# Kernel tuning notes

Measured on AMD Instinct MI355X. Metric: run time of the kernel, lower is better.

Reference implementation:

```python
import jax, jax.numpy as jnp
import numpy as np

B, SD, SE = 4, 2048, 2048
HID, HID_ = 300, 512
N_HEADS = 8


def setup_inputs() -> dict:
    key = jax.random.key(0)
    ks = jax.random.split(key, 7)
    en = jax.random.normal(ks[0], (B, SE, HID), dtype=jnp.float32)
    de = jax.random.normal(ks[1], (B, SD, HID), dtype=jnp.float32)
    mask = jax.random.randint(ks[2], (1, 1, SD, SE), 0, 2).astype(jnp.bool_)
    WQ = jax.random.normal(ks[3], (HID, HID_), dtype=jnp.float32)
    WK = jax.random.normal(ks[4], (HID, HID_), dtype=jnp.float32)
    WV = jax.random.normal(ks[5], (HID, HID_), dtype=jnp.float32)
    WO = jax.random.normal(ks[6], (HID_, HID), dtype=jnp.float32)
    return {"en": en, "de": de, "mask": mask, "WQ": WQ, "WK": WK, "WV": WV, "WO": WO}


def reference(en, de, mask, WQ, WK, WV, WO):
    # Faithful to the torch module (dropout in eval mode => identity).
    d_k = de.shape[-1]  # NOTE: original scales by sqrt(hidden_dim)=sqrt(300), not head_dim
    b_d, s_d = de.shape[0], de.shape[1]
    b_e, s_e = en.shape[0], en.shape[1]
    # head axis is the LAST axis of the reshape (size 8), exactly as the original view/permute
    q = jnp.transpose((de @ WQ).reshape(b_d, s_d, -1, N_HEADS), (3, 0, 1, 2))  # [8,B,Sd,64]
    k = jnp.transpose((en @ WK).reshape(b_e, s_e, -1, N_HEADS), (3, 0, 2, 1))  # [8,B,64,Se]
    v = jnp.transpose((en @ WV).reshape(b_e, s_e, -1, N_HEADS), (3, 0, 1, 2))  # [8,B,Se,64]
    e = jnp.matmul(q, k) / jnp.sqrt(jnp.asarray(d_k, dtype=q.dtype))           # [8,B,Sd,Se]
    e = jnp.where(mask, jnp.asarray(-1e9, dtype=e.dtype), e)
    alpha = jax.nn.softmax(e, axis=3)
    head3 = jnp.matmul(alpha, v)                                               # [8,B,Sd,64]
    # torch.cat((head3[0],...,head3[7]), 2) == move head axis into feature concat order
    a = jnp.concatenate([head3[h] for h in range(N_HEADS)], axis=2)            # [B,Sd,512]
    return a @ WO                                                              # [B,Sd,300]
```

## Files before the change

kernel.cpp:

```cpp
#include <hip/hip_runtime.h>
#include <hip/hip_bf16.h>
#include <math.h>

#define B_      4
#define SD_     2048
#define SE_     2048
#define HIDIN   300
#define HIDMID  512
#define NH      8
#define DH      64
#define ESZ     ((size_t)4194304)
#define BUFB    24576

typedef __attribute__((ext_vector_type(8))) short          s16x8;
typedef __attribute__((ext_vector_type(8))) unsigned short u16x8;
typedef __attribute__((ext_vector_type(4))) unsigned short u16x4;
typedef __attribute__((ext_vector_type(4))) float          f32x4;

#define MFMA16 __builtin_amdgcn_mfma_f32_16x16x32_bf16

#define QSCALE  0.0832940411f
#define NEGL   -1.4426950e9f
#define DEFER_THR 24.0f

__device__ __forceinline__ unsigned short f2bf(float f) {
    unsigned int u = __float_as_uint(f);
    u += 0x7fffu + ((u >> 16) & 1u);
    return (unsigned short)(u >> 16);
}
__device__ __forceinline__ float bf2f(unsigned short s) {
    return __uint_as_float((unsigned int)s << 16);
}
__device__ __forceinline__ void gload16(const void* g, void* l) {
    __builtin_amdgcn_global_load_lds(
        (const __attribute__((address_space(1))) void*)g,
        (__attribute__((address_space(3))) void*)l, 16, 0, 0);
}

#define OF_QH   ((size_t)0)
#define OF_QL   (ESZ)
#define OF_KH   (2*ESZ)
#define OF_KL   (3*ESZ)
#define OF_VT   (4*ESZ)
#define OF_CA   (5*ESZ)
#define OF_CW   (OF_CA + 10485760)
#define OF_WOT  (OF_CW + 983040)

__global__ __launch_bounds__(256) void bias_kernel(const int* __restrict__ mask,
                                                   unsigned int* __restrict__ BiasT)
{
    const int idx = blockIdx.x * 256 + threadIdx.x;
    const int q = idx >> 5, tile = idx & 31;
    const int* __restrict__ mrow = mask + (size_t)q * SE_ + tile * 64;
    const unsigned int NEGB = (unsigned int)f2bf(NEGL);
    const int qblk = q >> 4, qlo = q & 15;
#pragma unroll
    for (int g = 0; g < 4; ++g) {
        unsigned int w[8];
#pragma unroll
        for (int sub = 0; sub < 4; ++sub) {
            const int4 mm = *(const int4*)(mrow + sub * 16 + g * 4);
            w[sub * 2]     = (mm.x ? NEGB : 0u) | ((mm.y ? NEGB : 0u) << 16);
            w[sub * 2 + 1] = (mm.z ? NEGB : 0u) | ((mm.w ? NEGB : 0u) << 16);
        }
        unsigned int* dst = BiasT +
            ((((size_t)qblk * 32 + tile) * 4 + g) * 16 + qlo) * 8;
        *(uint4*)dst       = make_uint4(w[0], w[1], w[2], w[3]);
        *(uint4*)(dst + 4) = make_uint4(w[4], w[5], w[6], w[7]);
    }
}

__global__ __launch_bounds__(256) void convA_kernel(
    const float* __restrict__ de, const float* __restrict__ en,
    unsigned short* __restrict__ CA)
{
    const int idx = blockIdx.x * 256 + threadIdx.x;
    const int mat = blockIdx.y;
    const float* __restrict__ A = mat ? en : de;
    unsigned short* __restrict__ H = CA + (size_t)mat * 5242880;
    unsigned short* __restrict__ L = H + 2621440;
    const int row = idx / 10, ch = idx - row * 10;
    float v[32];
    if (ch < 9) {
#pragma unroll
        for (int i = 0; i < 8; ++i) {
            const float4 f = *(const float4*)(A + (size_t)row * 300 + ch * 32 + i * 4);
            v[i*4+0] = f.x; v[i*4+1] = f.y; v[i*4+2] = f.z; v[i*4+3] = f.w;
        }
    } else {
#pragma unroll
        for (int i = 0; i < 32; ++i) {
            const int k = 288 + i;
            v[i] = (k < 300) ? A[(size_t)row * 300 + k] : 0.f;
        }
    }
    const int r128 = row & 127;
    const int xr = (r128 >> 1) & 3;
    const size_t tb = ((size_t)(row >> 7) * 10 + ch) * 4096 + r128 * 32;
#pragma unroll
    for (int sub = 0; sub < 4; ++sub) {
        const int slot = sub ^ xr;
        u16x8 hv, lv;
#pragma unroll
        for (int e = 0; e < 8; ++e) {
            const float f = v[sub * 8 + e];
            const unsigned short h = f2bf(f);
            hv[e] = h; lv[e] = f2bf(f - bf2f(h));
        }
        *(u16x8*)(H + tb + slot * 8) = hv;
        *(u16x8*)(L + tb + slot * 8) = lv;
    }
}

__global__ __launch_bounds__(256) void convW_kernel(
    const float* __restrict__ WQ, const float* __restrict__ WK,
    const float* __restrict__ WV, const float* __restrict__ WO,
    unsigned short* __restrict__ CW, unsigned short* __restrict__ WOT)
{
    const int idx = blockIdx.x * 256 + threadIdx.x;
    if (idx < 122880) {
        const int which = idx / 40960;
        const int rem = idx - which * 40960;
        const int k = rem >> 7;
        const int n0 = (rem & 127) * 4;
        const float* __restrict__ W = which == 0 ? WQ : (which == 1 ? WK : WV);
        unsigned short* __restrict__ H = CW + (size_t)which * 327680;
        unsigned short* __restrict__ L = H + 163840;
        const float sc = (which == 0) ? QSCALE : 1.f;
        float4 w = make_float4(0.f, 0.f, 0.f, 0.f);
        if (k < 300) w = *(const float4*)(W + (size_t)k * 512 + n0);
        const float wv4[4] = {w.x * sc, w.y * sc, w.z * sc, w.w * sc};
        const int ch = k >> 5, kk = k & 31;
#pragma unroll
        for (int j = 0; j < 4; ++j) {
            const int n = n0 + j, ntile = n >> 7, nr = n & 127;
            const size_t o = ((size_t)(ntile * 10 + ch) * 128 + nr) * 32
                           + (((kk >> 3) ^ ((nr >> 1) & 3)) << 3) + (kk & 7);
            const unsigned short h = f2bf(wv4[j]);
            H[o] = h; L[o] = f2bf(wv4[j] - bf2f(h));
        }
    } else {
        const int idx2 = idx - 122880;
        const int k = idx2 / 96, n4 = idx2 - k * 96;
        const int n0 = n4 * 4;
        float4 w = make_float4(0.f, 0.f, 0.f, 0.f);
        if (n0 < 300) w = *(const float4*)(WO + (size_t)k * 300 + n0);
        const float wv4[4] = {w.x, w.y, w.z, w.w};
        const int ch = k >> 5, kk = k & 31;
#pragma unroll
        for (int j = 0; j < 4; ++j) {
            const int n = n0 + j, ntile = n >> 7, nr = n & 127;
            const size_t o = ((size_t)(ntile * 16 + ch) * 128 + nr) * 32
                           + (((kk >> 3) ^ ((nr >> 1) & 3)) << 3) + (kk & 7);
            WOT[o] = f2bf(wv4[j]);
        }
    }
}

__global__ __launch_bounds__(256) void proj_mfma_kernel(
    const unsigned short* __restrict__ CA, const unsigned short* __restrict__ CW,
    unsigned short* __restrict__ Qh, unsigned short* __restrict__ Ql,
    unsigned short* __restrict__ KhT, unsigned short* __restrict__ KlT,
    unsigned short* __restrict__ VtT)
{
    const int stile = blockIdx.x, jtile = blockIdx.y, which = blockIdx.z;
    const int tid = threadIdx.x, wv = tid >> 6, lane = tid & 63;
    const int li = lane & 15, g = lane >> 4;
    const int wr = wv >> 1, wc = wv & 1;

    __shared__ __align__(16) char LBp[65536];

    const unsigned short* __restrict__ pAh =
        CA + (size_t)(which ? 1 : 0) * 5242880 + (size_t)stile * 40960 + tid * 8;
    const unsigned short* __restrict__ pAl = pAh + 2621440;
    const unsigned short* __restrict__ pWh =
        CW + (size_t)which * 327680 + (size_t)jtile * 40960 + tid * 8;
    const unsigned short* __restrict__ pWl = pWh + 163840;

#define STAGEP(ch, bofs) {                                                    \
        char* db = LBp + (bofs) + wv * 1024;                                  \
        const size_t co = (size_t)(ch) * 4096;                                \
        gload16(pAh + co,        db);                                         \
        gload16(pAh + co + 2048, db + 4096);                                  \
        gload16(pAl + co,        db + 8192);                                  \
        gload16(pAl + co + 2048, db + 12288);                                 \
        gload16(pWh + co,        db + 16384);                                 \
        gload16(pWh + co + 2048, db + 20480);                                 \
        gload16(pWl + co,        db + 24576);                                 \
        gload16(pWl + co + 2048, db + 28672);                                 \
    }

    int offA[4], offW[4];
#pragma unroll
    for (int ssub = 0; ssub < 4; ++ssub) {
        const int r = wr * 64 + ssub * 16 + li;
        offA[ssub] = r * 64 + ((g ^ ((r >> 1) & 3)) << 4);
    }
#pragma unroll
    for (int jsub = 0; jsub < 4; ++jsub) {
        const int n = wc * 64 + jsub * 16 + li;
        offW[jsub] = n * 64 + ((g ^ ((n >> 1) & 3)) << 4);
    }

    f32x4 acc[4][4];
#pragma unroll
    for (int i = 0; i < 4; ++i)
#pragma unroll
        for (int j = 0; j < 4; ++j) acc[i][j] = (f32x4){0.f, 0.f, 0.f, 0.f};

    STAGEP(0, 0)
    __syncthreads();

#pragma unroll 1
    for (int ch = 0; ch < 10; ++ch) {
        const int bofs = (ch & 1) * 32768;
        if (ch < 9) STAGEP(ch + 1, bofs ^ 32768)
        const char* bp = LBp + bofs;
        s16x8 ah[4], al[4], wh[4], wl[4];
#pragma unroll
        for (int ssub = 0; ssub < 4; ++ssub) {
            ah[ssub] = *(const s16x8*)(bp + offA[ssub]);
            al[ssub] = *(const s16x8*)(bp + 8192 + offA[ssub]);
        }
#pragma unroll
        for (int jsub = 0; jsub < 4; ++jsub) {
            wh[jsub] = *(const s16x8*)(bp + 16384 + offW[jsub]);
            wl[jsub] = *(const s16x8*)(bp + 24576 + offW[jsub]);
        }
        __builtin_amdgcn_s_setprio(1);
#pragma unroll
        for (int ssub = 0; ssub < 4; ++ssub)
#pragma unroll
            for (int jsub = 0; jsub < 4; ++jsub) {
                acc[ssub][jsub] = MFMA16(ah[ssub], wh[jsub], acc[ssub][jsub], 0, 0, 0);
                acc[ssub][jsub] = MFMA16(ah[ssub], wl[jsub], acc[ssub][jsub], 0, 0, 0);
                acc[ssub][jsub] = MFMA16(al[ssub], wh[jsub], acc[ssub][jsub], 0, 0, 0);
            }
        __builtin_amdgcn_s_setprio(0);
        __syncthreads();
    }
#undef STAGEP

    const int jgbase = jtile * 128 + wc * 64 + li;
    const int sbase0 = stile * 128 + wr * 64 + 4 * g;
#pragma unroll
    for (int jsub = 0; jsub < 4; ++jsub) {
        const int jgg = jgbase + jsub * 16;
        const int d = jgg >> 3, hh = jgg & 7;
#pragma unroll
        for (int ssub = 0; ssub < 4; ++ssub) {
            const f32x4 v = acc[ssub][jsub];
            const int sg0 = sbase0 + ssub * 16;
            const int bbv = sg0 >> 11;
            const int bhn = bbv * 8 + hh;
            const int sl0 = sg0 & 2047;
            if (which == 0) {
                const size_t o = ((size_t)bhn * 2048 + sl0) * 64 + d;
#pragma unroll
                for (int r = 0; r < 4; ++r) {
                    const float val = v[r];
                    const unsigned short hi = f2bf(val);
                    Qh[o + r * 64] = hi;
                    Ql[o + r * 64] = f2bf(val - bf2f(hi));
                }
            } else if (which == 1) {
                const int tile = sl0 >> 6, tt0 = sl0 & 63;
                const size_t tb = ((size_t)(bhn * 32 + tile)) << 12;
#pragma unroll
                for (int r = 0; r < 4; ++r) {
                    const int tt = tt0 + r;
                    const size_t o = tb + tt * 64 + (((d >> 3) ^ (tt & 7)) << 3) + (d & 7);
                    const float val = v[r];
                    const unsigned short hi = f2bf(val);
                    KhT[o] = hi;
                    KlT[o] = f2bf(val - bf2f(hi));
                }
            } else {
                const int tile = sl0 >> 6, tin0 = sl0 & 63;
                const size_t tb = ((size_t)(bhn * 32 + tile)) << 12;
                const int blk = tin0 >> 5, gg2 = (tin0 >> 2) & 3, half = (tin0 >> 4) & 1;
                const size_t o = tb + (size_t)d * 64
                               + ((((blk << 2) | gg2) ^ (d & 7)) << 3) + half * 4;
                u16x4 pk;
#pragma unroll
                for (int r = 0; r < 4; ++r) pk[r] = f2bf(v[r]);
                *(u16x4*)(VtT + o) = pk;
            }
        }
    }
}

__global__ __launch_bounds__(256, 2) void attn_mfma_kernel(
    const unsigned short* __restrict__ Qh, const unsigned short* __restrict__ Ql,
    const unsigned short* __restrict__ KhT, const unsigned short* __restrict__ KlT,
    const unsigned short* __restrict__ VtT, const unsigned int* __restrict__ BiasT,
    unsigned short* __restrict__ AOb)
{
    const int lin = blockIdx.x + 16 * blockIdx.y;
    const int qt = (lin >> 3) & 15;
    const int bh = (lin & 7) + ((lin >> 7) << 3);
    const int bb = bh >> 3, hh = bh & 7;
    const int tid = threadIdx.x;
    const int wv = tid >> 6, lane = tid & 63;
    const int g = lane >> 4, li = lane & 15;
    const int q0r = qt * 128 + wv * 16 + li;

    __shared__ __align__(16) char LB[3 * BUFB];

    const size_t qoff = ((size_t)bh * SD_ + q0r) * DH + 8 * g;
    const s16x8 qh0_0 = *(const s16x8*)(Qh + qoff);
    const s16x8 qh1_0 = *(const s16x8*)(Qh + qoff + 32);
    const s16x8 ql0_0 = *(const s16x8*)(Ql + qoff);
    const s16x8 ql1_0 = *(const s16x8*)(Ql + qoff + 32);
    const s16x8 qh0_1 = *(const s16x8*)(Qh + qoff + 4096);
    const s16x8 qh1_1 = *(const s16x8*)(Qh + qoff + 4128);
    const s16x8 ql0_1 = *(const s16x8*)(Ql + qoff + 4096);
    const s16x8 ql1_1 = *(const s16x8*)(Ql + qoff + 4128);

    const unsigned short* __restrict__ sKh = KhT + ((size_t)bh << 17) + tid * 8;
    const unsigned short* __restrict__ sKl = KlT + ((size_t)bh << 17) + tid * 8;
    const unsigned short* __restrict__ sVt = VtT + ((size_t)bh << 17) + tid * 8;

    const int base0 = li * 128 + ((g ^ (li & 7)) << 4);
    const int base1 = li * 128 + (((4 + g) ^ (li & 7)) << 4);

    const size_t bb0 = ((((size_t)(qt * 8 + 0 * 4 + wv)) * 32) * 4 + g) * 16 * 8 + li * 8;
    const size_t bb1 = ((((size_t)(qt * 8 + 1 * 4 + wv)) * 32) * 4 + g) * 16 * 8 + li * 8;
#define BIASLOAD(T, R0A, R0B, R1A, R1B) {                                     \
        const uint4* p0 = (const uint4*)(BiasT + bb0 + (size_t)(T) * 512);    \
        R0A = p0[0]; R0B = p0[1];                                             \
        const uint4* p1 = (const uint4*)(BiasT + bb1 + (size_t)(T) * 512);    \
        R1A = p1[0]; R1B = p1[1];                                             \
    }

#define STAGE(tile, boff)                                                     \
    {                                                                         \
        char* db = LB + (boff) + wv * 1024;                                   \
        const size_t toff = (size_t)(tile) << 12;                             \
        gload16(sKh + toff,        db);                                       \
        gload16(sKh + toff + 2048, db + 4096);                                \
        gload16(sKl + toff,        db + 8192);                                \
        gload16(sKl + toff + 2048, db + 12288);                               \
        gload16(sVt + toff,        db + 16384);                               \
        gload16(sVt + toff + 2048, db + 20480);                               \
    }

    float m0 = -INFINITY, m1 = -INFINITY;
    f32x4 O0[4], O1[4], lacc0, lacc1;
#pragma unroll
    for (int i = 0; i < 4; ++i) {
        O0[i] = (f32x4){0.f, 0.f, 0.f, 0.f};
        O1[i] = (f32x4){0.f, 0.f, 0.f, 0.f};
    }
    lacc0 = (f32x4){0.f, 0.f, 0.f, 0.f};
    lacc1 = (f32x4){0.f, 0.f, 0.f, 0.f};

    s16x8 ones;
#pragma unroll
    for (int i = 0; i < 8; ++i) ones[i] = (short)0x3F80;

    uint4 cA0, cA1, cB0, cB1;
    uint4 nA0, nA1, nB0, nB1;

    STAGE(0, 0)
    BIASLOAD(0, cA0, cA1, cB0, cB1)
    STAGE(1, BUFB)
    asm volatile("s_waitcnt vmcnt(6)" ::: "memory");
    __builtin_amdgcn_s_barrier();
    __builtin_amdgcn_sched_barrier(0);

    int cc = 0, cs = 2 * BUFB;

#define UNPK(W, S, sub, cbase)                                                \
        S[sub][cbase]     = __uint_as_float((W) << 16);                       \
        S[sub][cbase + 1] = __uint_as_float((W) & 0xFFFF0000u);

#define ITER(IT, C0A, C0B, C1A, C1B, N0A, N0B, N1A, N1B)                      \
    {                                                                         \
        f32x4 s0[4], s1[4];                                                   \
        UNPK(C0A.x, s0, 0, 0) UNPK(C0A.y, s0, 0, 2)                           \
        UNPK(C0A.z, s0, 1, 0) UNPK(C0A.w, s0, 1, 2)                           \
        UNPK(C0B.x, s0, 2, 0) UNPK(C0B.y, s0, 2, 2)                           \
        UNPK(C0B.z, s0, 3, 0) UNPK(C0B.w, s0, 3, 2)                           \
        UNPK(C1A.x, s1, 0, 0) UNPK(C1A.y, s1, 0, 2)                           \
        UNPK(C1A.z, s1, 1, 0) UNPK(C1A.w, s1, 1, 2)                           \
        UNPK(C1B.x, s1, 2, 0) UNPK(C1B.y, s1, 2, 2)                           \
        UNPK(C1B.z, s1, 3, 0) UNPK(C1B.w, s1, 3, 2)                           \
        BIASLOAD(((IT) + 1) & 31, N0A, N0B, N1A, N1B)                         \
        __builtin_amdgcn_s_setprio(1);                                        \
        _Pragma("unroll")                                                     \
        for (int sub = 0; sub < 4; ++sub) {                                   \
            const s16x8 kh0 = *(const s16x8*)(LB + cc + base0 + sub * 2048);  \
            const s16x8 kh1 = *(const s16x8*)(LB + cc + base1 + sub * 2048);  \
            const s16x8 kl0 = *(const s16x8*)(LB + cc + base0 + 8192 + sub * 2048); \
            const s16x8 kl1 = *(const s16x8*)(LB + cc + base1 + 8192 + sub * 2048); \
            s0[sub] = MFMA16(kh0, qh0_0, s0[sub], 0, 0, 0);                   \
            s0[sub] = MFMA16(kh0, ql0_0, s0[sub], 0, 0, 0);                   \
            s0[sub] = MFMA16(kl0, qh0_0, s0[sub], 0, 0, 0);                   \
            s0[sub] = MFMA16(kh1, qh1_0, s0[sub], 0, 0, 0);                   \
            s0[sub] = MFMA16(kh1, ql1_0, s0[sub], 0, 0, 0);                   \
            s0[sub] = MFMA16(kl1, qh1_0, s0[sub], 0, 0, 0);                   \
            s1[sub] = MFMA16(kh0, qh0_1, s1[sub], 0, 0, 0);                   \
            s1[sub] = MFMA16(kh0, ql0_1, s1[sub], 0, 0, 0);                   \
            s1[sub] = MFMA16(kl0, qh0_1, s1[sub], 0, 0, 0);                   \
            s1[sub] = MFMA16(kh1, qh1_1, s1[sub], 0, 0, 0);                   \
            s1[sub] = MFMA16(kh1, ql1_1, s1[sub], 0, 0, 0);                   \
            s1[sub] = MFMA16(kl1, qh1_1, s1[sub], 0, 0, 0);                   \
        }                                                                     \
        __builtin_amdgcn_s_setprio(0);                                        \
        float t0, t1;                                                         \
        {                                                                     \
            float a = fmaxf(s0[0][0], fmaxf(s0[0][1], s0[0][2]));             \
            float b = fmaxf(s0[0][3], fmaxf(s0[1][0], s0[1][1]));             \
            float c = fmaxf(s0[1][2], fmaxf(s0[1][3], s0[2][0]));             \
            float d = fmaxf(s0[2][1], fmaxf(s0[2][2], s0[2][3]));             \
            float e = fmaxf(s0[3][0], fmaxf(s0[3][1], s0[3][2]));             \
            t0 = fmaxf(fmaxf(a, fmaxf(b, c)), fmaxf(s0[3][3], fmaxf(d, e)));  \
        }                                                                     \
        {                                                                     \
            float a = fmaxf(s1[0][0], fmaxf(s1[0][1], s1[0][2]));             \
            float b = fmaxf(s1[0][3], fmaxf(s1[1][0], s1[1][1]));             \
            float c = fmaxf(s1[1][2], fmaxf(s1[1][3], s1[2][0]));             \
            float d = fmaxf(s1[2][1], fmaxf(s1[2][2], s1[2][3]));             \
            float e = fmaxf(s1[3][0], fmaxf(s1[3][1], s1[3][2]));             \
            t1 = fmaxf(fmaxf(a, fmaxf(b, c)), fmaxf(s1[3][3], fmaxf(d, e)));  \
        }                                                                     \
        const int okd = (t0 <= m0 + DEFER_THR) && (t1 <= m1 + DEFER_THR);     \
        if (!__all(okd)) {                                                    \
            float r0 = fmaxf(t0, __shfl_xor(t0, 16));                         \
            r0 = fmaxf(r0, __shfl_xor(r0, 32));                               \
            float r1 = fmaxf(t1, __shfl_xor(t1, 16));                         \
            r1 = fmaxf(r1, __shfl_xor(r1, 32));                               \
            const float mn0 = fmaxf(m0, r0), mn1 = fmaxf(m1, r1);             \
            const float sc0 = exp2f(m0 - mn0), sc1 = exp2f(m1 - mn1);         \
            m0 = mn0; m1 = mn1;                                               \
            _Pragma("unroll")                                                 \
            for (int i = 0; i < 4; ++i) { O0[i] *= sc0; O1[i] *= sc1; }       \
            lacc0 *= sc0; lacc1 *= sc1;                                       \
        }                                                                     \
        _Pragma("unroll")                                                     \
        for (int sub = 0; sub < 4; ++sub)                                     \
            _Pragma("unroll")                                                 \
            for (int c = 0; c < 4; ++c) {                                     \
                s0[sub][c] = exp2f(s0[sub][c] - m0);                          \
                s1[sub][c] = exp2f(s1[sub][c] - m1);                          \
            }                                                                 \
        union { s16x8 v; unsigned int w[4]; } P00, P10, P01, P11;             \
        asm("v_cvt_pk_bf16_f32 %0, %1, %2" : "=v"(P00.w[0]) : "v"(s0[0][0]), "v"(s0[0][1])); \
        asm("v_cvt_pk_bf16_f32 %0, %1, %2" : "=v"(P00.w[1]) : "v"(s0[0][2]), "v"(s0[0][3])); \
        asm("v_cvt_pk_bf16_f32 %0, %1, %2" : "=v"(P00.w[2]) : "v"(s0[1][0]), "v"(s0[1][1])); \
        asm("v_cvt_pk_bf16_f32 %0, %1, %2" : "=v"(P00.w[3]) : "v"(s0[1][2]), "v"(s0[1][3])); \
        asm("v_cvt_pk_bf16_f32 %0, %1, %2" : "=v"(P10.w[0]) : "v"(s0[2][0]), "v"(s0[2][1])); \
        asm("v_cvt_pk_bf16_f32 %0, %1, %2" : "=v"(P10.w[1]) : "v"(s0[2][2]), "v"(s0[2][3])); \
        asm("v_cvt_pk_bf16_f32 %0, %1, %2" : "=v"(P10.w[2]) : "v"(s0[3][0]), "v"(s0[3][1])); \
        asm("v_cvt_pk_bf16_f32 %0, %1, %2" : "=v"(P10.w[3]) : "v"(s0[3][2]), "v"(s0[3][3])); \
        asm("v_cvt_pk_bf16_f32 %0, %1, %2" : "=v"(P01.w[0]) : "v"(s1[0][0]), "v"(s1[0][1])); \
        asm("v_cvt_pk_bf16_f32 %0, %1, %2" : "=v"(P01.w[1]) : "v"(s1[0][2]), "v"(s1[0][3])); \
        asm("v_cvt_pk_bf16_f32 %0, %1, %2" : "=v"(P01.w[2]) : "v"(s1[1][0]), "v"(s1[1][1])); \
        asm("v_cvt_pk_bf16_f32 %0, %1, %2" : "=v"(P01.w[3]) : "v"(s1[1][2]), "v"(s1[1][3])); \
        asm("v_cvt_pk_bf16_f32 %0, %1, %2" : "=v"(P11.w[0]) : "v"(s1[2][0]), "v"(s1[2][1])); \
        asm("v_cvt_pk_bf16_f32 %0, %1, %2" : "=v"(P11.w[1]) : "v"(s1[2][2]), "v"(s1[2][3])); \
        asm("v_cvt_pk_bf16_f32 %0, %1, %2" : "=v"(P11.w[2]) : "v"(s1[3][0]), "v"(s1[3][1])); \
        asm("v_cvt_pk_bf16_f32 %0, %1, %2" : "=v"(P11.w[3]) : "v"(s1[3][2]), "v"(s1[3][3])); \
        __builtin_amdgcn_s_setprio(1);                                        \
        _Pragma("unroll")                                                     \
        for (int dsub = 0; dsub < 4; ++dsub) {                                \
            const s16x8 vf0 = *(const s16x8*)(LB + cc + base0 + 16384 + dsub * 2048); \
            const s16x8 vf1 = *(const s16x8*)(LB + cc + base1 + 16384 + dsub * 2048); \
            O0[dsub] = MFMA16(vf0, P00.v, O0[dsub], 0, 0, 0);                 \
            O0[dsub] = MFMA16(vf1, P10.v, O0[dsub], 0, 0, 0);                 \
            O1[dsub] = MFMA16(vf0, P01.v, O1[dsub], 0, 0, 0);                 \
            O1[dsub] = MFMA16(vf1, P11.v, O1[dsub], 0, 0, 0);                 \
        }                                                                     \
        lacc0 = MFMA16(ones, P00.v, lacc0, 0, 0, 0);                          \
        lacc0 = MFMA16(ones, P10.v, lacc0, 0, 0, 0);                          \
        lacc1 = MFMA16(ones, P01.v, lacc1, 0, 0, 0);                          \
        lacc1 = MFMA16(ones, P11.v, lacc1, 0, 0, 0);                          \
        __builtin_amdgcn_s_setprio(0);                                        \
        STAGE(((IT) + 2) & 31, cs)                                            \
        asm volatile("s_waitcnt vmcnt(6)" ::: "memory");                      \
        __builtin_amdgcn_s_barrier();                                         \
        __builtin_amdgcn_sched_barrier(0);                                    \
        cc += BUFB; if (cc == 3 * BUFB) cc = 0;                               \
        cs += BUFB; if (cs == 3 * BUFB) cs = 0;                               \
    }

#pragma unroll 1
    for (int itp = 0; itp < 32; itp += 2) {
        ITER(itp,     cA0, cA1, cB0, cB1, nA0, nA1, nB0, nB1)
        ITER(itp + 1, nA0, nA1, nB0, nB1, cA0, cA1, cB0, cB1)
    }

#pragma unroll
    for (int qs = 0; qs < 2; ++qs) {
        const float rl = 1.f / (qs ? lacc1[0] : lacc0[0]);
        const f32x4* Oq = qs ? O1 : O0;
        const int row = bb * 2048 + qt * 128 + qs * 64 + wv * 16 + li;
        const int r128 = row & 127;
        const int xr = (r128 >> 1) & 3;
        unsigned short* __restrict__ ab = AOb + ((size_t)(row >> 7)) * 65536
                                        + r128 * 32 + (g & 1) * 4;
#pragma unroll
        for (int dsub = 0; dsub < 4; ++dsub) {
            const f32x4 o = Oq[dsub] * rl;
            const int ch = hh * 2 + (dsub >> 1);
            const int slot = ((dsub & 1) * 2 + (g >> 1)) ^ xr;
            u16x4 pk;
#pragma unroll
            for (int c = 0; c < 4; ++c) pk[c] = f2bf(o[c]);
            *(u16x4*)(ab + (size_t)ch * 4096 + slot * 8) = pk;
        }
    }
#undef STAGE
#undef BIASLOAD
#undef UNPK
#undef ITER
}

__global__ __launch_bounds__(256) void epi_mfma_kernel(
    const unsigned short* __restrict__ AOb, const unsigned short* __restrict__ WOT,
    float* __restrict__ out)
{
    const int stile = blockIdx.x, jtile = blockIdx.y;
    const int tid = threadIdx.x, wv = tid >> 6, lane = tid & 63;
    const int li = lane & 15, g = lane >> 4;

    __shared__ __align__(16) char LBe[24576];

    const unsigned short* __restrict__ pA =
        AOb + (size_t)(stile >> 1) * 65536 + (stile & 1) * 2048 + tid * 8;
    const unsigned short* __restrict__ pW = WOT + (size_t)jtile * 65536 + tid * 8;

#define STAGEE(ch, bofs) {                                                    \
        char* dbA = LBe + (bofs) + wv * 1024;                                 \
        const size_t co = (size_t)(ch) * 4096;                                \
        gload16(pA + co,        dbA);                                         \
        gload16(pW + co,        dbA + 4096);                                  \
        gload16(pW + co + 2048, dbA + 8192);                                  \
    }

    int offA[4], offW[2];
#pragma unroll
    for (int ssub = 0; ssub < 4; ++ssub) {
        const int r = ssub * 16 + li;
        offA[ssub] = r * 64 + ((g ^ ((r >> 1) & 3)) << 4);
    }
#pragma unroll
    for (int jsub = 0; jsub < 2; ++jsub) {
        const int n = wv * 32 + jsub * 16 + li;
        offW[jsub] = 4096 + n * 64 + ((g ^ ((n >> 1) & 3)) << 4);
    }

    f32x4 acc[4][2];
#pragma unroll
    for (int i = 0; i < 4; ++i)
#pragma unroll
        for (int j = 0; j < 2; ++j) acc[i][j] = (f32x4){0.f, 0.f, 0.f, 0.f};

    STAGEE(0, 0)
    __syncthreads();

#pragma unroll 1
    for (int ch = 0; ch < 16; ++ch) {
        const int bofs = (ch & 1) * 12288;
        if (ch < 15) STAGEE(ch + 1, bofs ^ 12288)
        const char* bp = LBe + bofs;
        s16x8 ah[4], wh[2];
#pragma unroll
        for (int ssub = 0; ssub < 4; ++ssub)
            ah[ssub] = *(const s16x8*)(bp + offA[ssub]);
#pragma unroll
        for (int jsub = 0; jsub < 2; ++jsub)
            wh[jsub] = *(const s16x8*)(bp + offW[jsub]);
        __builtin_amdgcn_s_setprio(1);
#pragma unroll
        for (int ssub = 0; ssub < 4; ++ssub)
#pragma unroll
            for (int jsub = 0; jsub < 2; ++jsub)
                acc[ssub][jsub] = MFMA16(ah[ssub], wh[jsub], acc[ssub][jsub], 0, 0, 0);
        __builtin_amdgcn_s_setprio(0);
        __syncthreads();
    }
#undef STAGEE

    const int nbase = jtile * 128 + wv * 32 + li;
    const int rbase = stile * 64 + 4 * g;
#pragma unroll
    for (int jsub = 0; jsub < 2; ++jsub) {
        const int o = nbase + jsub * 16;
        if (o < HIDIN) {
#pragma unroll
            for (int ssub = 0; ssub < 4; ++ssub) {
                const f32x4 v = acc[ssub][jsub];
                const int r0 = rbase + ssub * 16;
#pragma unroll
                for (int r = 0; r < 4; ++r)
                    out[(size_t)(r0 + r) * HIDIN + o] = v[r];
            }
        }
    }
}

extern "C" void kernel_launch(void* const* d_in, const int* in_sizes, int n_in,
                              void* d_out, int out_size, void* d_ws, size_t ws_size,
                              hipStream_t stream)
{
    const float* en  = (const float*)d_in[0];
    const float* de  = (const float*)d_in[1];
    const int*   mask = (const int*)d_in[2];
    const float* WQ  = (const float*)d_in[3];
    const float* WK  = (const float*)d_in[4];
    const float* WV  = (const float*)d_in[5];
    const float* WO  = (const float*)d_in[6];
    float* out = (float*)d_out;

    unsigned short* ws2 = (unsigned short*)d_ws;
    unsigned short* Qh  = ws2 + OF_QH;
    unsigned short* Ql  = ws2 + OF_QL;
    unsigned short* KhT = ws2 + OF_KH;
    unsigned short* KlT = ws2 + OF_KL;
    unsigned short* VtT = ws2 + OF_VT;
    unsigned short* CA  = ws2 + OF_CA;
    unsigned short* CW  = ws2 + OF_CW;
    unsigned short* WOT = ws2 + OF_WOT;
    unsigned short* AOb = CA;
    unsigned int*  BiasT = (unsigned int*)(CA + 4194304);

    convA_kernel<<<dim3(320, 2), 256, 0, stream>>>(de, en, CA);
    convW_kernel<<<dim3(672), 256, 0, stream>>>(WQ, WK, WV, WO, CW, WOT);
    proj_mfma_kernel<<<dim3(64, 4, 3), 256, 0, stream>>>(CA, CW, Qh, Ql, KhT, KlT, VtT);
    bias_kernel<<<dim3(256), 256, 0, stream>>>(mask, BiasT);
    attn_mfma_kernel<<<dim3(16, 32), 256, 0, stream>>>(Qh, Ql, KhT, KlT, VtT, BiasT, AOb);
    epi_mfma_kernel<<<dim3(128, 3), 256, 0, stream>>>(AOb, WOT, out);
}
```

Measured before the change: 187.8 us.

## Double attention block to 8 waves and software-pipeline QK with softmax-PV

The attention kernel now uses 512-thread blocks covering 256 query rows, so each staged K/V tile in LDS is shared by twice as many waves, and the LDS ring grows from three to four buffers. The loop is software-pipelined so the QK^T MFMAs for tile i+1 are issued alongside the softmax and PV work for tile i, with a prologue and epilogue added. The aim is to halve K/V global traffic per query and hide the exp/convert latency behind tensor-core work. In exchange it needs more registers for two live score sets and more LDS, which may lower occupancy below the two blocks per CU requested.

```diff
diff --git a/kernel.cpp b/kernel.cpp
--- a/kernel.cpp
+++ b/kernel.cpp
@@ -290,32 +290,33 @@
     }
 }
 
-__global__ __launch_bounds__(256, 2) void attn_mfma_kernel(
+__global__ __launch_bounds__(512, 2) void attn_mfma_kernel(
     const unsigned short* __restrict__ Qh, const unsigned short* __restrict__ Ql,
     const unsigned short* __restrict__ KhT, const unsigned short* __restrict__ KlT,
     const unsigned short* __restrict__ VtT, const unsigned int* __restrict__ BiasT,
     unsigned short* __restrict__ AOb)
 {
-    const int lin = blockIdx.x + 16 * blockIdx.y;
-    const int qt = (lin >> 3) & 15;
-    const int bh = (lin & 7) + ((lin >> 7) << 3);
+    const int lin = blockIdx.x + 8 * blockIdx.y;
+    const int j = lin >> 3;
+    const int qt = j & 7;
+    const int bh = (lin & 7) + ((j >> 3) << 3);
     const int bb = bh >> 3, hh = bh & 7;
     const int tid = threadIdx.x;
     const int wv = tid >> 6, lane = tid & 63;
     const int g = lane >> 4, li = lane & 15;
-    const int q0r = qt * 128 + wv * 16 + li;
-
-    __shared__ __align__(16) char LB[3 * BUFB];
+    const int q0r = qt * 256 + wv * 16 + li;
+
+    __shared__ __align__(16) char LB[4 * BUFB];
 
     const size_t qoff = ((size_t)bh * SD_ + q0r) * DH + 8 * g;
     const s16x8 qh0_0 = *(const s16x8*)(Qh + qoff);
     const s16x8 qh1_0 = *(const s16x8*)(Qh + qoff + 32);
     const s16x8 ql0_0 = *(const s16x8*)(Ql + qoff);
     const s16x8 ql1_0 = *(const s16x8*)(Ql + qoff + 32);
-    const s16x8 qh0_1 = *(const s16x8*)(Qh + qoff + 4096);
-    const s16x8 qh1_1 = *(const s16x8*)(Qh + qoff + 4128);
-    const s16x8 ql0_1 = *(const s16x8*)(Ql + qoff + 4096);
-    const s16x8 ql1_1 = *(const s16x8*)(Ql + qoff + 4128);
+    const s16x8 qh0_1 = *(const s16x8*)(Qh + qoff + 8192);
+    const s16x8 qh1_1 = *(const s16x8*)(Qh + qoff + 8224);
+    const s16x8 ql0_1 = *(const s16x8*)(Ql + qoff + 8192);
+    const s16x8 ql1_1 = *(const s16x8*)(Ql + qoff + 8224);
 
     const unsigned short* __restrict__ sKh = KhT + ((size_t)bh << 17) + tid * 8;
     const unsigned short* __restrict__ sKl = KlT + ((size_t)bh << 17) + tid * 8;
@@ -324,8 +325,9 @@
     const int base0 = li * 128 + ((g ^ (li & 7)) << 4);
     const int base1 = li * 128 + (((4 + g) ^ (li & 7)) << 4);
 
-    const size_t bb0 = ((((size_t)(qt * 8 + 0 * 4 + wv)) * 32) * 4 + g) * 16 * 8 + li * 8;
-    const size_t bb1 = ((((size_t)(qt * 8 + 1 * 4 + wv)) * 32) * 4 + g) * 16 * 8 + li * 8;
+    const size_t bb0 = (((size_t)(qt * 16 + wv) * 32) * 4 + g) * 128 + li * 8;
+    const size_t bb1 = (((size_t)(qt * 16 + 8 + wv) * 32) * 4 + g) * 128 + li * 8;
+
 #define BIASLOAD(T, R0A, R0B, R1A, R1B) {                                     \
         const uint4* p0 = (const uint4*)(BiasT + bb0 + (size_t)(T) * 512);    \
         R0A = p0[0]; R0B = p0[1];                                             \
@@ -337,12 +339,9 @@
     {                                                                         \
         char* db = LB + (boff) + wv * 1024;                                   \
         const size_t toff = (size_t)(tile) << 12;                             \
-        gload16(sKh + toff,        db);                                       \
-        gload16(sKh + toff + 2048, db + 4096);                                \
-        gload16(sKl + toff,        db + 8192);                                \
-        gload16(sKl + toff + 2048, db + 12288);                               \
-        gload16(sVt + toff,        db + 16384);                               \
-        gload16(sVt + toff + 2048, db + 20480);                               \
+        gload16(sKh + toff, db);                                              \
+        gload16(sKl + toff, db + 8192);                                       \
+        gload16(sVt + toff, db + 16384);                                      \
     }
 
     float m0 = -INFINITY, m1 = -INFINITY;
@@ -359,34 +358,24 @@
 #pragma unroll
     for (int i = 0; i < 8; ++i) ones[i] = (short)0x3F80;
 
+    f32x4 sA0[4], sA1[4], sB0[4], sB1[4];
     uint4 cA0, cA1, cB0, cB1;
     uint4 nA0, nA1, nB0, nB1;
-
-    STAGE(0, 0)
-    BIASLOAD(0, cA0, cA1, cB0, cB1)
-    STAGE(1, BUFB)
-    asm volatile("s_waitcnt vmcnt(6)" ::: "memory");
-    __builtin_amdgcn_s_barrier();
-    __builtin_amdgcn_sched_barrier(0);
-
-    int cc = 0, cs = 2 * BUFB;
 
 #define UNPK(W, S, sub, cbase)                                                \
         S[sub][cbase]     = __uint_as_float((W) << 16);                       \
         S[sub][cbase + 1] = __uint_as_float((W) & 0xFFFF0000u);
 
-#define ITER(IT, C0A, C0B, C1A, C1B, N0A, N0B, N1A, N1B)                      \
+#define SBLOCK(S0, S1, BA0, BA1, BB0, BB1)                                    \
     {                                                                         \
-        f32x4 s0[4], s1[4];                                                   \
-        UNPK(C0A.x, s0, 0, 0) UNPK(C0A.y, s0, 0, 2)                           \
-        UNPK(C0A.z, s0, 1, 0) UNPK(C0A.w, s0, 1, 2)                           \
-        UNPK(C0B.x, s0, 2, 0) UNPK(C0B.y, s0, 2, 2)                           \
-        UNPK(C0B.z, s0, 3, 0) UNPK(C0B.w, s0, 3, 2)                           \
-        UNPK(C1A.x, s1, 0, 0) UNPK(C1A.y, s1, 0, 2)                           \
-        UNPK(C1A.z, s1, 1, 0) UNPK(C1A.w, s1, 1, 2)                           \
-        UNPK(C1B.x, s1, 2, 0) UNPK(C1B.y, s1, 2, 2)                           \
-        UNPK(C1B.z, s1, 3, 0) UNPK(C1B.w, s1, 3, 2)                           \
-        BIASLOAD(((IT) + 1) & 31, N0A, N0B, N1A, N1B)                         \
+        UNPK(BA0.x, S0, 0, 0) UNPK(BA0.y, S0, 0, 2)                           \
+        UNPK(BA0.z, S0, 1, 0) UNPK(BA0.w, S0, 1, 2)                           \
+        UNPK(BA1.x, S0, 2, 0) UNPK(BA1.y, S0, 2, 2)                           \
+        UNPK(BA1.z, S0, 3, 0) UNPK(BA1.w, S0, 3, 2)                           \
+        UNPK(BB0.x, S1, 0, 0) UNPK(BB0.y, S1, 0, 2)                           \
+        UNPK(BB0.z, S1, 1, 0) UNPK(BB0.w, S1, 1, 2)                           \
+        UNPK(BB1.x, S1, 2, 0) UNPK(BB1.y, S1, 2, 2)                           \
+        UNPK(BB1.z, S1, 3, 0) UNPK(BB1.w, S1, 3, 2)                           \
         __builtin_amdgcn_s_setprio(1);                                        \
         _Pragma("unroll")                                                     \
         for (int sub = 0; sub < 4; ++sub) {                                   \
@@ -394,36 +383,40 @@
             const s16x8 kh1 = *(const s16x8*)(LB + cc + base1 + sub * 2048);  \
             const s16x8 kl0 = *(const s16x8*)(LB + cc + base0 + 8192 + sub * 2048); \
             const s16x8 kl1 = *(const s16x8*)(LB + cc + base1 + 8192 + sub * 2048); \
-            s0[sub] = MFMA16(kh0, qh0_0, s0[sub], 0, 0, 0);                   \
-            s0[sub] = MFMA16(kh0, ql0_0, s0[sub], 0, 0, 0);                   \
-            s0[sub] = MFMA16(kl0, qh0_0, s0[sub], 0, 0, 0);                   \
-            s0[sub] = MFMA16(kh1, qh1_0, s0[sub], 0, 0, 0);                   \
-            s0[sub] = MFMA16(kh1, ql1_0, s0[sub], 0, 0, 0);                   \
-            s0[sub] = MFMA16(kl1, qh1_0, s0[sub], 0, 0, 0);                   \
-            s1[sub] = MFMA16(kh0, qh0_1, s1[sub], 0, 0, 0);                   \
-            s1[sub] = MFMA16(kh0, ql0_1, s1[sub], 0, 0, 0);                   \
-            s1[sub] = MFMA16(kl0, qh0_1, s1[sub], 0, 0, 0);                   \
-            s1[sub] = MFMA16(kh1, qh1_1, s1[sub], 0, 0, 0);                   \
-            s1[sub] = MFMA16(kh1, ql1_1, s1[sub], 0, 0, 0);                   \
-            s1[sub] = MFMA16(kl1, qh1_1, s1[sub], 0, 0, 0);                   \
+            S0[sub] = MFMA16(kh0, qh0_0, S0[sub], 0, 0, 0);                   \
+            S0[sub] = MFMA16(kh0, ql0_0, S0[sub], 0, 0, 0);                   \
+            S0[sub] = MFMA16(kl0, qh0_0, S0[sub], 0, 0, 0);                   \
+            S0[sub] = MFMA16(kh1, qh1_0, S0[sub], 0, 0, 0);                   \
+            S0[sub] = MFMA16(kh1, ql1_0, S0[sub], 0, 0, 0);                   \
+            S0[sub] = MFMA16(kl1, qh1_0, S0[sub], 0, 0, 0);                   \
+            S1[sub] = MFMA16(kh0, qh0_1, S1[sub], 0, 0, 0);                   \
+            S1[sub] = MFMA16(kh0, ql0_1, S1[sub], 0, 0, 0);                   \
+            S1[sub] = MFMA16(kl0, qh0_1, S1[sub], 0, 0, 0);                   \
+            S1[sub] = MFMA16(kh1, qh1_1, S1[sub], 0, 0, 0);                   \
+            S1[sub] = MFMA16(kh1, ql1_1, S1[sub], 0, 0, 0);                   \
+            S1[sub] = MFMA16(kl1, qh1_1, S1[sub], 0, 0, 0);                   \
         }                                                                     \
         __builtin_amdgcn_s_setprio(0);                                        \
+    }
+
+#define SMPV(S0, S1)                                                          \
+    {                                                                         \
         float t0, t1;                                                         \
         {                                                                     \
-            float a = fmaxf(s0[0][0], fmaxf(s0[0][1], s0[0][2]));             \
-            float b = fmaxf(s0[0][3], fmaxf(s0[1][0], s0[1][1]));             \
-            float c = fmaxf(s0[1][2], fmaxf(s0[1][3], s0[2][0]));             \
-            float d = fmaxf(s0[2][1], fmaxf(s0[2][2], s0[2][3]));             \
-            float e = fmaxf(s0[3][0], fmaxf(s0[3][1], s0[3][2]));             \
-            t0 = fmaxf(fmaxf(a, fmaxf(b, c)), fmaxf(s0[3][3], fmaxf(d, e)));  \
+            float a = fmaxf(S0[0][0], fmaxf(S0[0][1], S0[0][2]));             \
+            float b = fmaxf(S0[0][3], fmaxf(S0[1][0], S0[1][1]));             \
+            float c = fmaxf(S0[1][2], fmaxf(S0[1][3], S0[2][0]));             \
+            float d = fmaxf(S0[2][1], fmaxf(S0[2][2], S0[2][3]));             \
+            float e = fmaxf(S0[3][0], fmaxf(S0[3][1], S0[3][2]));             \
+            t0 = fmaxf(fmaxf(a, fmaxf(b, c)), fmaxf(S0[3][3], fmaxf(d, e)));  \
         }                                                                     \
         {                                                                     \
-            float a = fmaxf(s1[0][0], fmaxf(s1[0][1], s1[0][2]));             \
-            float b = fmaxf(s1[0][3], fmaxf(s1[1][0], s1[1][1]));             \
-            float c = fmaxf(s1[1][2], fmaxf(s1[1][3], s1[2][0]));             \
-            float d = fmaxf(s1[2][1], fmaxf(s1[2][2], s1[2][3]));             \
-            float e = fmaxf(s1[3][0], fmaxf(s1[3][1], s1[3][2]));             \
-            t1 = fmaxf(fmaxf(a, fmaxf(b, c)), fmaxf(s1[3][3], fmaxf(d, e)));  \
+            float a = fmaxf(S1[0][0], fmaxf(S1[0][1], S1[0][2]));             \
+            float b = fmaxf(S1[0][3], fmaxf(S1[1][0], S1[1][1]));             \
+            float c = fmaxf(S1[1][2], fmaxf(S1[1][3], S1[2][0]));             \
+            float d = fmaxf(S1[2][1], fmaxf(S1[2][2], S1[2][3]));             \
+            float e = fmaxf(S1[3][0], fmaxf(S1[3][1], S1[3][2]));             \
+            t1 = fmaxf(fmaxf(a, fmaxf(b, c)), fmaxf(S1[3][3], fmaxf(d, e)));  \
         }                                                                     \
         const int okd = (t0 <= m0 + DEFER_THR) && (t1 <= m1 + DEFER_THR);     \
         if (!__all(okd)) {                                                    \
@@ -442,31 +435,31 @@
         for (int sub = 0; sub < 4; ++sub)                                     \
             _Pragma("unroll")                                                 \
             for (int c = 0; c < 4; ++c) {                                     \
-                s0[sub][c] = exp2f(s0[sub][c] - m0);                          \
-                s1[sub][c] = exp2f(s1[sub][c] - m1);                          \
+                S0[sub][c] = exp2f(S0[sub][c] - m0);                          \
+                S1[sub][c] = exp2f(S1[sub][c] - m1);                          \
             }                                                                 \
         union { s16x8 v; unsigned int w[4]; } P00, P10, P01, P11;             \
-        asm("v_cvt_pk_bf16_f32 %0, %1, %2" : "=v"(P00.w[0]) : "v"(s0[0][0]), "v"(s0[0][1])); \
-        asm("v_cvt_pk_bf16_f32 %0, %1, %2" : "=v"(P00.w[1]) : "v"(s0[0][2]), "v"(s0[0][3])); \
-        asm("v_cvt_pk_bf16_f32 %0, %1, %2" : "=v"(P00.w[2]) : "v"(s0[1][0]), "v"(s0[1][1])); \
-        asm("v_cvt_pk_bf16_f32 %0, %1, %2" : "=v"(P00.w[3]) : "v"(s0[1][2]), "v"(s0[1][3])); \
-        asm("v_cvt_pk_bf16_f32 %0, %1, %2" : "=v"(P10.w[0]) : "v"(s0[2][0]), "v"(s0[2][1])); \
-        asm("v_cvt_pk_bf16_f32 %0, %1, %2" : "=v"(P10.w[1]) : "v"(s0[2][2]), "v"(s0[2][3])); \
-        asm("v_cvt_pk_bf16_f32 %0, %1, %2" : "=v"(P10.w[2]) : "v"(s0[3][0]), "v"(s0[3][1])); \
-        asm("v_cvt_pk_bf16_f32 %0, %1, %2" : "=v"(P10.w[3]) : "v"(s0[3][2]), "v"(s0[3][3])); \
-        asm("v_cvt_pk_bf16_f32 %0, %1, %2" : "=v"(P01.w[0]) : "v"(s1[0][0]), "v"(s1[0][1])); \
-        asm("v_cvt_pk_bf16_f32 %0, %1, %2" : "=v"(P01.w[1]) : "v"(s1[0][2]), "v"(s1[0][3])); \
-        asm("v_cvt_pk_bf16_f32 %0, %1, %2" : "=v"(P01.w[2]) : "v"(s1[1][0]), "v"(s1[1][1])); \
-        asm("v_cvt_pk_bf16_f32 %0, %1, %2" : "=v"(P01.w[3]) : "v"(s1[1][2]), "v"(s1[1][3])); \
-        asm("v_cvt_pk_bf16_f32 %0, %1, %2" : "=v"(P11.w[0]) : "v"(s1[2][0]), "v"(s1[2][1])); \
-        asm("v_cvt_pk_bf16_f32 %0, %1, %2" : "=v"(P11.w[1]) : "v"(s1[2][2]), "v"(s1[2][3])); \
-        asm("v_cvt_pk_bf16_f32 %0, %1, %2" : "=v"(P11.w[2]) : "v"(s1[3][0]), "v"(s1[3][1])); \
-        asm("v_cvt_pk_bf16_f32 %0, %1, %2" : "=v"(P11.w[3]) : "v"(s1[3][2]), "v"(s1[3][3])); \
+        asm("v_cvt_pk_bf16_f32 %0, %1, %2" : "=v"(P00.w[0]) : "v"(S0[0][0]), "v"(S0[0][1])); \
+        asm("v_cvt_pk_bf16_f32 %0, %1, %2" : "=v"(P00.w[1]) : "v"(S0[0][2]), "v"(S0[0][3])); \
+        asm("v_cvt_pk_bf16_f32 %0, %1, %2" : "=v"(P00.w[2]) : "v"(S0[1][0]), "v"(S0[1][1])); \
+        asm("v_cvt_pk_bf16_f32 %0, %1, %2" : "=v"(P00.w[3]) : "v"(S0[1][2]), "v"(S0[1][3])); \
+        asm("v_cvt_pk_bf16_f32 %0, %1, %2" : "=v"(P10.w[0]) : "v"(S0[2][0]), "v"(S0[2][1])); \
+        asm("v_cvt_pk_bf16_f32 %0, %1, %2" : "=v"(P10.w[1]) : "v"(S0[2][2]), "v"(S0[2][3])); \
+        asm("v_cvt_pk_bf16_f32 %0, %1, %2" : "=v"(P10.w[2]) : "v"(S0[3][0]), "v"(S0[3][1])); \
+        asm("v_cvt_pk_bf16_f32 %0, %1, %2" : "=v"(P10.w[3]) : "v"(S0[3][2]), "v"(S0[3][3])); \
+        asm("v_cvt_pk_bf16_f32 %0, %1, %2" : "=v"(P01.w[0]) : "v"(S1[0][0]), "v"(S1[0][1])); \
+        asm("v_cvt_pk_bf16_f32 %0, %1, %2" : "=v"(P01.w[1]) : "v"(S1[0][2]), "v"(S1[0][3])); \
+        asm("v_cvt_pk_bf16_f32 %0, %1, %2" : "=v"(P01.w[2]) : "v"(S1[1][0]), "v"(S1[1][1])); \
+        asm("v_cvt_pk_bf16_f32 %0, %1, %2" : "=v"(P01.w[3]) : "v"(S1[1][2]), "v"(S1[1][3])); \
+        asm("v_cvt_pk_bf16_f32 %0, %1, %2" : "=v"(P11.w[0]) : "v"(S1[2][0]), "v"(S1[2][1])); \
+        asm("v_cvt_pk_bf16_f32 %0, %1, %2" : "=v"(P11.w[1]) : "v"(S1[2][2]), "v"(S1[2][3])); \
+        asm("v_cvt_pk_bf16_f32 %0, %1, %2" : "=v"(P11.w[2]) : "v"(S1[3][0]), "v"(S1[3][1])); \
+        asm("v_cvt_pk_bf16_f32 %0, %1, %2" : "=v"(P11.w[3]) : "v"(S1[3][2]), "v"(S1[3][3])); \
         __builtin_amdgcn_s_setprio(1);                                        \
         _Pragma("unroll")                                                     \
         for (int dsub = 0; dsub < 4; ++dsub) {                                \
-            const s16x8 vf0 = *(const s16x8*)(LB + cc + base0 + 16384 + dsub * 2048); \
-            const s16x8 vf1 = *(const s16x8*)(LB + cc + base1 + 16384 + dsub * 2048); \
+            const s16x8 vf0 = *(const s16x8*)(LB + cp + base0 + 16384 + dsub * 2048); \
+            const s16x8 vf1 = *(const s16x8*)(LB + cp + base1 + 16384 + dsub * 2048); \
             O0[dsub] = MFMA16(vf0, P00.v, O0[dsub], 0, 0, 0);                 \
             O0[dsub] = MFMA16(vf1, P10.v, O0[dsub], 0, 0, 0);                 \
             O1[dsub] = MFMA16(vf0, P01.v, O1[dsub], 0, 0, 0);                 \
@@ -477,25 +470,55 @@
         lacc1 = MFMA16(ones, P01.v, lacc1, 0, 0, 0);                          \
         lacc1 = MFMA16(ones, P11.v, lacc1, 0, 0, 0);                          \
         __builtin_amdgcn_s_setprio(0);                                        \
-        STAGE(((IT) + 2) & 31, cs)                                            \
-        asm volatile("s_waitcnt vmcnt(6)" ::: "memory");                      \
+    }
+
+#define ENDITER                                                               \
+        asm volatile("s_waitcnt vmcnt(7)" ::: "memory");                      \
         __builtin_amdgcn_s_barrier();                                         \
         __builtin_amdgcn_sched_barrier(0);                                    \
-        cc += BUFB; if (cc == 3 * BUFB) cc = 0;                               \
-        cs += BUFB; if (cs == 3 * BUFB) cs = 0;                               \
-    }
+        cp = cc; cc += BUFB; if (cc == 4 * BUFB) cc = 0;                      \
+        cs += BUFB; if (cs == 4 * BUFB) cs = 0;
+
+#define ITER(IT, SC0, SC1, SP0, SP1, CA0_, CA1_, CB0_, CB1_, NA0_, NA1_, NB0_, NB1_) \
+    {                                                                         \
+        STAGE(((IT) + 2) & 31, cs)                                            \
+        SBLOCK(SC0, SC1, CA0_, CA1_, CB0_, CB1_)                              \
+        BIASLOAD(((IT) + 1) & 31, NA0_, NA1_, NB0_, NB1_)                     \
+        SMPV(SP0, SP1)                                                        \
+        ENDITER                                                               \
+    }
+
+    int cc = 0, cp = 0, cs = 2 * BUFB;
+
+    BIASLOAD(0, cA0, cA1, cB0, cB1)
+    STAGE(0, 0)
+    STAGE(1, BUFB)
+    asm volatile("s_waitcnt vmcnt(3)" ::: "memory");
+    __builtin_amdgcn_s_barrier();
+    __builtin_amdgcn_sched_barrier(0);
+
+    STAGE(2, cs)
+    SBLOCK(sA0, sA1, cA0, cA1, cB0, cB1)
+    BIASLOAD(1, nA0, nA1, nB0, nB1)
+    asm volatile("s_waitcnt vmcnt(7)" ::: "memory");
+    __builtin_amdgcn_s_barrier();
+    __builtin_amdgcn_sched_barrier(0);
+    cp = 0; cc = BUFB; cs = 3 * BUFB;
 
 #pragma unroll 1
-    for (int itp = 0; itp < 32; itp += 2) {
-        ITER(itp,     cA0, cA1, cB0, cB1, nA0, nA1, nB0, nB1)
-        ITER(itp + 1, nA0, nA1, nB0, nB1, cA0, cA1, cB0, cB1)
-    }
+    for (int it = 1; it < 31; it += 2) {
+        ITER(it,     sB0, sB1, sA0, sA1, nA0, nA1, nB0, nB1, cA0, cA1, cB0, cB1)
+        ITER(it + 1, sA0, sA1, sB0, sB1, cA0, cA1, cB0, cB1, nA0, nA1, nB0, nB1)
+    }
+    ITER(31, sB0, sB1, sA0, sA1, nA0, nA1, nB0, nB1, cA0, cA1, cB0, cB1)
+
+    SMPV(sB0, sB1)
 
 #pragma unroll
     for (int qs = 0; qs < 2; ++qs) {
         const float rl = 1.f / (qs ? lacc1[0] : lacc0[0]);
         const f32x4* Oq = qs ? O1 : O0;
-        const int row = bb * 2048 + qt * 128 + qs * 64 + wv * 16 + li;
+        const int row = bb * 2048 + qt * 256 + qs * 128 + wv * 16 + li;
         const int r128 = row & 127;
         const int xr = (r128 >> 1) & 3;
         unsigned short* __restrict__ ab = AOb + ((size_t)(row >> 7)) * 65536
@@ -514,6 +537,9 @@
 #undef STAGE
 #undef BIASLOAD
 #undef UNPK
+#undef SBLOCK
+#undef SMPV
+#undef ENDITER
 #undef ITER
 }
 
@@ -630,6 +656,6 @@
     convW_kernel<<<dim3(672), 256, 0, stream>>>(WQ, WK, WV, WO, CW, WOT);
     proj_mfma_kernel<<<dim3(64, 4, 3), 256, 0, stream>>>(CA, CW, Qh, Ql, KhT, KlT, VtT);
     bias_kernel<<<dim3(256), 256, 0, stream>>>(mask, BiasT);
-    attn_mfma_kernel<<<dim3(16, 32), 256, 0, stream>>>(Qh, Ql, KhT, KlT, VtT, BiasT, AOb);
+    attn_mfma_kernel<<<dim3(8, 32), 512, 0, stream>>>(Qh, Ql, KhT, KlT, VtT, BiasT, AOb);
     epi_mfma_kernel<<<dim3(128, 3), 256, 0, stream>>>(AOb, WOT, out);
 }
```

Measured after the change: 192.5 us. 1.03x slower.
